# Kernel tuning notes

Measured on AMD Instinct MI355X. Metric: run time of the kernel, lower is better.

## Reference

```python
import jax, jax.numpy as jnp
import numpy as np

HEADS = 8
DIM_HEAD = 64
BOTTLENECK = 40


def setup_inputs() -> dict:
    key = jax.random.key(0)
    ks = jax.random.split(key, 10)
    b, n, qs = 4, 1024, 256
    inner = HEADS * DIM_HEAD
    s = lambda fan_in: 1.0 / np.sqrt(fan_in)
    return {
        "x":   jax.random.normal(ks[0], (b, n, qs), dtype=jnp.float32),
        # weights stored as (in, out) so forward is x @ W
        "wq1": jax.random.normal(ks[1], (qs, BOTTLENECK), dtype=jnp.float32) * s(qs),
        "wq2": jax.random.normal(ks[2], (BOTTLENECK, inner), dtype=jnp.float32) * s(BOTTLENECK),
        "wk1": jax.random.normal(ks[3], (qs, BOTTLENECK), dtype=jnp.float32) * s(qs),
        "wk2": jax.random.normal(ks[4], (BOTTLENECK, inner), dtype=jnp.float32) * s(BOTTLENECK),
        "wv1": jax.random.normal(ks[5], (qs, BOTTLENECK), dtype=jnp.float32) * s(qs),
        "wv2": jax.random.normal(ks[6], (BOTTLENECK, inner), dtype=jnp.float32) * s(BOTTLENECK),
        "wo":  jax.random.normal(ks[7], (inner, qs), dtype=jnp.float32) * s(inner),
        "bo":  jax.random.normal(ks[8], (qs,), dtype=jnp.float32) * 0.01,
    }


def reference(x, wq1, wq2, wk1, wk2, wv1, wv2, wo, bo):
    b, n, _ = x.shape
    h, d = HEADS, DIM_HEAD
    scale = d ** -0.5

    # bottlenecked QKV projections (40-dim), SiLU on K bottleneck
    q = (x @ wq1) @ wq2                       # (b, n, h*d)
    k = jax.nn.silu(x @ wk1) @ wk2            # (b, n, h*d)
    v = (x @ wv1) @ wv2                       # (b, n, h*d)

    def split(t):  # 'b n (h d) -> b (h n) d'
        return t.reshape(b, n, h, d).transpose(0, 2, 1, 3).reshape(b, h * n, d)

    q, k, v = split(q), split(k), split(v)

    sim = jnp.einsum('bid,bjd->bij', q, k) * scale   # (b, h*n, h*n)
    attn = jax.nn.softmax(sim, axis=-1)
    out = jnp.einsum('bij,bjd->bid', attn, v)        # (b, h*n, d)

    # 'b (h n) d -> b n (h d)'
    out = out.reshape(b, h, n, d).transpose(0, 2, 1, 3).reshape(b, n, h * d)
    return out @ wo + bo
```

## Files before the change

kernel.cpp:

```cpp
#include <hip/hip_runtime.h>
#include <hip/hip_bf16.h>


#define B_    4
#define H_    8
#define NSEQ  1024
#define SEQ   8192
#define DH    64
#define QS    256
#define INNER 512
#define QSCALE 0.18033688011112042f

#define KVSW_BATCH 524288
#define OPHALF (2097152)

typedef __bf16 bf16x8 __attribute__((ext_vector_type(8)));
typedef float floatx4 __attribute__((ext_vector_type(4)));

__global__ __launch_bounds__(512, 4) void qkv_kernel(
    const float* __restrict__ x,
    const float* __restrict__ wq1, const float* __restrict__ wq2,
    const float* __restrict__ wk1, const float* __restrict__ wk2,
    const float* __restrict__ wv1, const float* __restrict__ wv2,
    const float* __restrict__ wo,
    __hip_bfloat16* __restrict__ Qg, __hip_bfloat16* __restrict__ KSg,
    __hip_bfloat16* __restrict__ VSg,
    __hip_bfloat16* __restrict__ WOBH, __hip_bfloat16* __restrict__ WOBL)
{
  const int tid  = threadIdx.x;

  if (blockIdx.x >= 768) {
    const int cid = blockIdx.x - 768;
    const int t4  = (cid * 512 + tid) * 4;
    const int n   = t4 & 255;
    const int k8  = t4 >> 8;
    float4 rr[8];
    #pragma unroll
    for (int kk = 0; kk < 8; ++kk)
      rr[kk] = *(const float4*)(wo + (size_t)(k8 * 8 + kk) * QS + n);
    const int kc = k8 >> 2, qq = k8 & 3;
    #pragma unroll
    for (int nn = 0; nn < 4; ++nn) {
      const int nc = n + nn;
      const int l  = (nc & 15) + 16 * qq;
      const size_t off = ((size_t)((nc >> 4) * 16 + kc) * 64 + l) * 8;
      bf16x8 hv, lv;
      #pragma unroll
      for (int kk = 0; kk < 8; ++kk) {
        const float v = (nn == 0) ? rr[kk].x : (nn == 1) ? rr[kk].y
                      : (nn == 2) ? rr[kk].z : rr[kk].w;
        const __bf16 h16 = (__bf16)v;
        hv[kk] = h16;
        lv[kk] = (__bf16)(v - (float)h16);
      }
      *(bf16x8*)(WOBH + off) = hv;
      *(bf16x8*)(WOBL + off) = lv;
    }
    return;
  }

  const int p    = blockIdx.x >> 8;
  const int rest = blockIdx.x & 255;
  const int b    = rest >> 6;
  const int nblk = rest & 63;
  const int n0   = nblk << 4;

  __shared__ __align__(16) float xs[16][260];
  __shared__ __align__(16) float tb2[4][16][40];
  __shared__ __align__(16) float tb[16][40];
  __shared__ __align__(16) __hip_bfloat16 ob[10400];

  const float* w1 = (p == 0) ? wq1 : (p == 1) ? wk1 : wv1;
  const float* w2 = (p == 0) ? wq2 : (p == 1) ? wk2 : wv2;

  #pragma unroll
  for (int j = 0; j < 2; ++j) {
    const int i  = tid + j * 512;
    const int r  = i >> 6;
    const int c4 = (i & 63) << 2;
    *(float4*)(&xs[r][c4]) =
        *(const float4*)(x + ((size_t)b * NSEQ + n0 + r) * QS + c4);
  }
  __syncthreads();

  for (int t = tid; t < 640; t += 512) {
    const int ks  = t / 160;
    const int rem = t - ks * 160;
    const int r   = rem / 10;
    const int bn  = (rem - r * 10) * 4;
    float a0 = 0.f, a1 = 0.f, a2 = 0.f, a3 = 0.f;
    #pragma unroll 4
    for (int c4 = ks * 16; c4 < ks * 16 + 16; ++c4) {
      const float4 xv = *(const float4*)(&xs[r][c4 * 4]);
      const float4 wa = *(const float4*)(w1 + (c4 * 4 + 0) * 40 + bn);
      const float4 wb = *(const float4*)(w1 + (c4 * 4 + 1) * 40 + bn);
      const float4 wc = *(const float4*)(w1 + (c4 * 4 + 2) * 40 + bn);
      const float4 wd = *(const float4*)(w1 + (c4 * 4 + 3) * 40 + bn);
      a0 += xv.x * wa.x + xv.y * wb.x + xv.z * wc.x + xv.w * wd.x;
      a1 += xv.x * wa.y + xv.y * wb.y + xv.z * wc.y + xv.w * wd.y;
      a2 += xv.x * wa.z + xv.y * wb.z + xv.z * wc.z + xv.w * wd.z;
      a3 += xv.x * wa.w + xv.y * wb.w + xv.z * wc.w + xv.w * wd.w;
    }
    tb2[ks][r][bn + 0] = a0; tb2[ks][r][bn + 1] = a1;
    tb2[ks][r][bn + 2] = a2; tb2[ks][r][bn + 3] = a3;
  }
  __syncthreads();

  if (tid < 160) {
    const int r  = tid / 10;
    const int bn = (tid - r * 10) * 4;
    const float4 h0 = *(const float4*)(&tb2[0][r][bn]);
    const float4 h1 = *(const float4*)(&tb2[1][r][bn]);
    const float4 h2 = *(const float4*)(&tb2[2][r][bn]);
    const float4 h3 = *(const float4*)(&tb2[3][r][bn]);
    float a0 = (h0.x + h1.x) + (h2.x + h3.x);
    float a1 = (h0.y + h1.y) + (h2.y + h3.y);
    float a2 = (h0.z + h1.z) + (h2.z + h3.z);
    float a3 = (h0.w + h1.w) + (h2.w + h3.w);
    if (p == 1) {
      a0 = a0 / (1.f + __expf(-a0));
      a1 = a1 / (1.f + __expf(-a1));
      a2 = a2 / (1.f + __expf(-a2));
      a3 = a3 / (1.f + __expf(-a3));
    }
    tb[r][bn + 0] = a0; tb[r][bn + 1] = a1;
    tb[r][bn + 2] = a2; tb[r][bn + 3] = a3;
  }
  __syncthreads();

  {
    const int cq = tid & 127;
    const int rq = tid >> 7;
    const int c  = cq * 4, r0 = rq * 4;
    const float scale = (p == 0) ? QSCALE : 1.0f;
    float acc[4][4];
    #pragma unroll
    for (int i = 0; i < 4; ++i)
      #pragma unroll
      for (int j = 0; j < 4; ++j) acc[i][j] = 0.f;

    #pragma unroll 2
    for (int jb = 0; jb < 10; ++jb) {
      const float4 w0  = *(const float4*)(w2 + (jb * 4 + 0) * INNER + c);
      const float4 w1r = *(const float4*)(w2 + (jb * 4 + 1) * INNER + c);
      const float4 w2r = *(const float4*)(w2 + (jb * 4 + 2) * INNER + c);
      const float4 w3  = *(const float4*)(w2 + (jb * 4 + 3) * INNER + c);
      #pragma unroll
      for (int ri = 0; ri < 4; ++ri) {
        const float4 tv = *(const float4*)(&tb[r0 + ri][jb * 4]);
        acc[ri][0] += tv.x * w0.x + tv.y * w1r.x + tv.z * w2r.x + tv.w * w3.x;
        acc[ri][1] += tv.x * w0.y + tv.y * w1r.y + tv.z * w2r.y + tv.w * w3.y;
        acc[ri][2] += tv.x * w0.z + tv.y * w1r.z + tv.z * w2r.z + tv.w * w3.z;
        acc[ri][3] += tv.x * w0.w + tv.y * w1r.w + tv.z * w2r.w + tv.w * w3.w;
      }
    }
    #pragma unroll
    for (int ri = 0; ri < 4; ++ri)
      #pragma unroll
      for (int ci = 0; ci < 4; ++ci) {
        const int cc = c + ci;
        const float v = acc[ri][ci] * scale;
        if (p == 2) ob[cc * 20 + r0 + ri]    = __float2bfloat16(v);
        else        ob[(r0 + ri) * 520 + cc] = __float2bfloat16(v);
      }
  }
  __syncthreads();

  if (p == 0) {
    #pragma unroll
    for (int j = 0; j < 2; ++j) {
      const int i  = tid + j * 512;
      const int h  = i >> 7;
      const int r  = (i >> 3) & 15;
      const int d8 = i & 7;
      *(float4*)(Qg + ((size_t)b * SEQ + h * NSEQ + n0 + r) * DH + d8 * 8) =
          *(const float4*)(&ob[r * 520 + h * 64 + d8 * 8]);
    }
  } else if (p == 1) {
    #pragma unroll
    for (int j = 0; j < 2; ++j) {
      const int i    = tid + j * 512;
      const int h    = i >> 7;
      const int ks2  = (i >> 6) & 1;
      const int quad = (i >> 4) & 3;
      const int r    = i & 15;
      const int lane = quad * 16 + r;
      const size_t dst = (size_t)b * KVSW_BATCH
          + ((size_t)((h * 64 + nblk) * 2 + ks2) * 64 + lane) * 8;
      *(float4*)(KSg + dst) = *(const float4*)(&ob[r * 520 + h * 64 + ks2 * 32 + quad * 8]);
    }
  } else {
    const int st  = nblk & 1;
    const int p32 = nblk >> 1;
    #pragma unroll
    for (int pass = 0; pass < 4; ++pass) {
      const int i   = tid + pass * 512;
      const int h   = i >> 8;
      const int dnt = (i >> 6) & 3;
      const int dm  = (i >> 2) & 15;
      const int rg  = i & 3;
      const int lane = rg * 16 + dm;
      const size_t dst = (size_t)b * KVSW_BATCH
          + ((size_t)((h * 32 + p32) * 4 + dnt) * 64 + lane) * 8 + st * 4;
      *(uint2*)(VSg + dst) = *(const uint2*)(&ob[(h * 64 + dnt * 16 + dm) * 20 + rg * 4]);
    }
  }
}

struct PairBuf {
  bf16x8 k[2][2];
  bf16x8 v[4];
};

__global__ __launch_bounds__(256, 3) void attn_kernel(
    const __hip_bfloat16* __restrict__ Qg,
    const __hip_bfloat16* __restrict__ KSg,
    const __hip_bfloat16* __restrict__ VSg,
    float* __restrict__ OPg,
    float* __restrict__ PSg)
{
  __shared__ float Osh[4][16][68];
  __shared__ float psums[4][64];

  const int tid  = threadIdx.x;
  const int wave = tid >> 6;
  const int lane = tid & 63;
  const int lrow = lane & 15;
  const int quad = lane >> 4;

  const int xcd   = blockIdx.x & 7;
  const int idx   = blockIdx.x >> 3;
  const int b     = xcd >> 1;
  const int half  = idx & 1;
  const int qtile = (xcd & 1) * 64 + (idx >> 1);
  const int qbase = qtile * 64;

  const __hip_bfloat16* Qb  = Qg + ((size_t)b * SEQ + qbase) * DH;
  const __hip_bfloat16* kp0 = KSg + (size_t)b * KVSW_BATCH + half * 262144
                              + (size_t)wave * 65536 + lane * 8;
  const __hip_bfloat16* vp0 = VSg + (size_t)b * KVSW_BATCH + half * 262144
                              + (size_t)wave * 65536 + lane * 8;

  bf16x8 qf[4][2];
  #pragma unroll
  for (int mt = 0; mt < 4; ++mt)
    #pragma unroll
    for (int s = 0; s < 2; ++s)
      qf[mt][s] = *(const bf16x8*)(Qb + (mt * 16 + lrow) * DH + s * 32 + quad * 8);

  floatx4 oacc[4][4];
  #pragma unroll
  for (int mt = 0; mt < 4; ++mt)
    #pragma unroll
    for (int dnt = 0; dnt < 4; ++dnt)
      oacc[mt][dnt] = (floatx4){0.f, 0.f, 0.f, 0.f};
  float psum[4] = {0.f, 0.f, 0.f, 0.f};

  #pragma unroll 2
  for (int pair = 0; pair < 32; ++pair) {
    PairBuf pb;
    const __hip_bfloat16* kp = kp0 + pair * 2048;
    pb.k[0][0] = *(const bf16x8*)(kp);
    pb.k[0][1] = *(const bf16x8*)(kp + 512);
    pb.k[1][0] = *(const bf16x8*)(kp + 1024);
    pb.k[1][1] = *(const bf16x8*)(kp + 1536);
    const __hip_bfloat16* vp = vp0 + pair * 2048;
    #pragma unroll
    for (int dnt = 0; dnt < 4; ++dnt)
      pb.v[dnt] = *(const bf16x8*)(vp + dnt * 512);

    #pragma unroll
    for (int mt = 0; mt < 4; ++mt) {
      floatx4 s0 = (floatx4){0.f, 0.f, 0.f, 0.f};
      floatx4 s1 = (floatx4){0.f, 0.f, 0.f, 0.f};
      s0 = __builtin_amdgcn_mfma_f32_16x16x32_bf16(pb.k[0][0], qf[mt][0], s0, 0, 0, 0);
      s0 = __builtin_amdgcn_mfma_f32_16x16x32_bf16(pb.k[0][1], qf[mt][1], s0, 0, 0, 0);
      s1 = __builtin_amdgcn_mfma_f32_16x16x32_bf16(pb.k[1][0], qf[mt][0], s1, 0, 0, 0);
      s1 = __builtin_amdgcn_mfma_f32_16x16x32_bf16(pb.k[1][1], qf[mt][1], s1, 0, 0, 0);
      float p[8];
      #pragma unroll
      for (int r = 0; r < 4; ++r) {
        p[r]     = __builtin_amdgcn_exp2f(s0[r]);
        p[4 + r] = __builtin_amdgcn_exp2f(s1[r]);
      }
      psum[mt] += ((p[0] + p[1]) + (p[2] + p[3])) + ((p[4] + p[5]) + (p[6] + p[7]));
      bf16x8 pa;
      #pragma unroll
      for (int j = 0; j < 8; ++j) pa[j] = (__bf16)p[j];
      #pragma unroll
      for (int dnt = 0; dnt < 4; ++dnt)
        oacc[mt][dnt] = __builtin_amdgcn_mfma_f32_16x16x32_bf16(pa, pb.v[dnt], oacc[mt][dnt], 0, 0, 0);
    }
  }

  #pragma unroll
  for (int mt = 0; mt < 4; ++mt) {
    float s = psum[mt];
    s += __shfl_xor(s, 16, 64);
    s += __shfl_xor(s, 32, 64);
    psum[mt] = s;
  }
  if (quad == 0) {
    #pragma unroll
    for (int mt = 0; mt < 4; ++mt)
      psums[wave][mt * 16 + lrow] = psum[mt];
  }

  const size_t opbase = ((size_t)half * B_ + b) * SEQ + qbase;

  #pragma unroll
  for (int mt = 0; mt < 4; ++mt) {
    #pragma unroll
    for (int dnt = 0; dnt < 4; ++dnt)
      #pragma unroll
      for (int r = 0; r < 4; ++r)
        Osh[wave][quad * 4 + r][dnt * 16 + lrow] = oacc[mt][dnt][r];
    __syncthreads();

    {
      const int q16 = tid >> 4;
      const int d0  = (tid & 15) * 4;
      float4 a0 = *(const float4*)(&Osh[0][q16][d0]);
      float4 a1 = *(const float4*)(&Osh[1][q16][d0]);
      float4 a2 = *(const float4*)(&Osh[2][q16][d0]);
      float4 a3 = *(const float4*)(&Osh[3][q16][d0]);
      float4 res;
      res.x = (a0.x + a1.x) + (a2.x + a3.x);
      res.y = (a0.y + a1.y) + (a2.y + a3.y);
      res.z = (a0.z + a1.z) + (a2.z + a3.z);
      res.w = (a0.w + a1.w) + (a2.w + a3.w);
      *(float4*)(OPg + (opbase + mt * 16 + q16) * DH + d0) = res;
    }
    if (mt == 0 && tid < 64) {
      const float tot = (psums[0][tid] + psums[1][tid]) + (psums[2][tid] + psums[3][tid]);
      PSg[opbase + tid] = tot;
    }
    __syncthreads();
  }
}

__global__ __launch_bounds__(256, 1) void out_kernel(
    const float* __restrict__ OPg, const float* __restrict__ PSg,
    const __hip_bfloat16* __restrict__ WOBH, const __hip_bfloat16* __restrict__ WOBL,
    const float* __restrict__ bo, float* __restrict__ out)
{
  __shared__ __align__(16) __hip_bfloat16 apH[8192];
  __shared__ __align__(16) __hip_bfloat16 apL[8192];
  __shared__ float invs[16][8];

  const int tid  = threadIdx.x;
  const int b    = blockIdx.x >> 6;
  const int n0   = (blockIdx.x & 63) << 4;
  const int lane = tid & 63;
  const int wave = tid >> 6;

  if (tid < 128) {
    const int r = tid >> 3, h = tid & 7;
    const size_t row = (size_t)b * SEQ + h * NSEQ + n0 + r;
    invs[r][h] = 1.0f / (PSg[row] + PSg[(size_t)B_ * SEQ + row]);
  }
  __syncthreads();

  {
    const int m   = tid & 15;
    const int q   = (tid >> 4) & 3;
    const int kc0 = tid >> 6;
    #pragma unroll
    for (int pss = 0; pss < 4; ++pss) {
      const int kc = kc0 + pss * 4;
      const int h  = kc >> 1;
      const int dh = (q + 4 * (kc & 1)) * 8;
      const size_t idx = (((size_t)b * H_ + h) * NSEQ + n0 + m) * DH + dh;
      const float4 a0 = *(const float4*)(OPg + idx);
      const float4 a1 = *(const float4*)(OPg + idx + 4);
      const float4 b0 = *(const float4*)(OPg + OPHALF + idx);
      const float4 b1 = *(const float4*)(OPg + OPHALF + idx + 4);
      const float inv = invs[m][h];
      float v[8];
      v[0] = (a0.x + b0.x) * inv; v[1] = (a0.y + b0.y) * inv;
      v[2] = (a0.z + b0.z) * inv; v[3] = (a0.w + b0.w) * inv;
      v[4] = (a1.x + b1.x) * inv; v[5] = (a1.y + b1.y) * inv;
      v[6] = (a1.z + b1.z) * inv; v[7] = (a1.w + b1.w) * inv;
      bf16x8 hv, lv;
      #pragma unroll
      for (int j = 0; j < 8; ++j) {
        const __bf16 h16 = (__bf16)v[j];
        hv[j] = h16;
        lv[j] = (__bf16)(v[j] - (float)h16);
      }
      const int off = (kc * 64 + (m + 16 * q)) * 8;
      *(bf16x8*)(apH + off) = hv;
      *(bf16x8*)(apL + off) = lv;
    }
  }
  __syncthreads();

  bf16x8 ah[16], al[16];
  #pragma unroll
  for (int kc = 0; kc < 16; ++kc) {
    ah[kc] = *(const bf16x8*)(apH + (kc * 64 + lane) * 8);
    al[kc] = *(const bf16x8*)(apL + (kc * 64 + lane) * 8);
  }

  const int colq = lane & 15;
  const int quad = lane >> 4;

  #pragma unroll
  for (int nt4 = 0; nt4 < 4; ++nt4) {
    const int nt = nt4 * 4 + wave;
    const __hip_bfloat16* wbh = WOBH + ((size_t)nt * 16 * 64 + lane) * 8;
    const __hip_bfloat16* wbl = WOBL + ((size_t)nt * 16 * 64 + lane) * 8;
    floatx4 aHH = (floatx4){0.f, 0.f, 0.f, 0.f};
    floatx4 aHL = (floatx4){0.f, 0.f, 0.f, 0.f};
    floatx4 aLH = (floatx4){0.f, 0.f, 0.f, 0.f};
    #pragma unroll
    for (int kg = 0; kg < 4; ++kg) {
      bf16x8 bh[4], bl[4];
      #pragma unroll
      for (int j = 0; j < 4; ++j) {
        bh[j] = *(const bf16x8*)(wbh + (kg * 4 + j) * 512);
        bl[j] = *(const bf16x8*)(wbl + (kg * 4 + j) * 512);
      }
      #pragma unroll
      for (int j = 0; j < 4; ++j) {
        const int kc = kg * 4 + j;
        aHH = __builtin_amdgcn_mfma_f32_16x16x32_bf16(ah[kc], bh[j], aHH, 0, 0, 0);
        aHL = __builtin_amdgcn_mfma_f32_16x16x32_bf16(ah[kc], bl[j], aHL, 0, 0, 0);
        aLH = __builtin_amdgcn_mfma_f32_16x16x32_bf16(al[kc], bh[j], aLH, 0, 0, 0);
      }
    }
    const int n  = nt * 16 + colq;
    const float bv = bo[n];
    #pragma unroll
    for (int r = 0; r < 4; ++r) {
      const int mm = quad * 4 + r;
      out[((size_t)b * NSEQ + n0 + mm) * QS + n] =
          ((aHH[r] + aHL[r]) + aLH[r]) + bv;
    }
  }
}

extern "C" void kernel_launch(void* const* d_in, const int* in_sizes, int n_in,
                              void* d_out, int out_size, void* d_ws, size_t ws_size,
                              hipStream_t stream) {
  const float* x   = (const float*)d_in[0];
  const float* wq1 = (const float*)d_in[1];
  const float* wq2 = (const float*)d_in[2];
  const float* wk1 = (const float*)d_in[3];
  const float* wk2 = (const float*)d_in[4];
  const float* wv1 = (const float*)d_in[5];
  const float* wv2 = (const float*)d_in[6];
  const float* wo  = (const float*)d_in[7];
  const float* bo  = (const float*)d_in[8];
  float* out = (float*)d_out;

  __hip_bfloat16* Qg  = (__hip_bfloat16*)d_ws;
  __hip_bfloat16* KSg = Qg + (size_t)B_ * SEQ * DH;
  __hip_bfloat16* VSg = KSg + (size_t)B_ * KVSW_BATCH;
  float*          OPg = (float*)(VSg + (size_t)B_ * KVSW_BATCH);
  float*          PSg = OPg + 2 * (size_t)B_ * SEQ * DH;
  __hip_bfloat16* WOBH = (__hip_bfloat16*)(PSg + 2 * (size_t)B_ * SEQ);
  __hip_bfloat16* WOBL = WOBH + (size_t)INNER * QS;

  qkv_kernel<<<776, 512, 0, stream>>>(x, wq1, wq2, wk1, wk2, wv1, wv2, wo,
                                      Qg, KSg, VSg, WOBH, WOBL);
  attn_kernel<<<1024, 256, 0, stream>>>(Qg, KSg, VSg, OPg, PSg);
  out_kernel<<<256, 256, 0, stream>>>(OPg, PSg, WOBH, WOBL, bo, out);
}
```

Baseline: 179.9 us.

## Move QKV bottleneck projections to split-bf16 MFMA with fused Q/K/V blocks

The QKV projection now runs both stages of the bottleneck GEMMs on bf16 MFMA instructions. A 3-term hi/lo split (hh + hl + lh) keeps accuracy close to fp32. A new conv_kernel converts all weight matrices into swizzled hi/lo bf16 layouts ahead of time. Each qkv block now computes Q, K and V together for its 16 rows, so x is loaded once instead of three times, and the grid drops from 768 to 256 blocks. The cost is an extra kernel launch and MFMA-layout overhead on very small matrices (40-wide bottleneck padded to 64), and fewer blocks means less parallelism.

```diff
diff --git a/kernel.cpp b/kernel.cpp
--- a/kernel.cpp
+++ b/kernel.cpp
@@ -17,21 +17,62 @@
 typedef __bf16 bf16x8 __attribute__((ext_vector_type(8)));
 typedef float floatx4 __attribute__((ext_vector_type(4)));
 
-__global__ __launch_bounds__(512, 4) void qkv_kernel(
-    const float* __restrict__ x,
-    const float* __restrict__ wq1, const float* __restrict__ wq2,
-    const float* __restrict__ wk1, const float* __restrict__ wk2,
-    const float* __restrict__ wv1, const float* __restrict__ wv2,
+__global__ __launch_bounds__(256) void conv_kernel(
+    const float* __restrict__ wq1, const float* __restrict__ wk1,
+    const float* __restrict__ wv1,
+    const float* __restrict__ wq2, const float* __restrict__ wk2,
+    const float* __restrict__ wv2,
     const float* __restrict__ wo,
-    __hip_bfloat16* __restrict__ Qg, __hip_bfloat16* __restrict__ KSg,
-    __hip_bfloat16* __restrict__ VSg,
+    __hip_bfloat16* __restrict__ W1BH, __hip_bfloat16* __restrict__ W1BL,
+    __hip_bfloat16* __restrict__ W2BH, __hip_bfloat16* __restrict__ W2BL,
     __hip_bfloat16* __restrict__ WOBH, __hip_bfloat16* __restrict__ WOBL)
 {
-  const int tid  = threadIdx.x;
-
-  if (blockIdx.x >= 768) {
-    const int cid = blockIdx.x - 768;
-    const int t4  = (cid * 512 + tid) * 4;
+  const int tid = threadIdx.x;
+  const int blk = blockIdx.x;
+
+  if (blk < 16) {
+    const int t  = blk * 256 + tid;
+    const int n  = t & 127;
+    const int kq = t >> 7;
+    const int kc = kq >> 2, q = kq & 3;
+    const float* src; int col;
+    if (n < 40)       { src = wq1; col = n; }
+    else if (n < 80)  { src = wk1; col = n - 40; }
+    else if (n < 120) { src = wv1; col = n - 80; }
+    else              { src = nullptr; col = 0; }
+    bf16x8 hv, lv;
+    #pragma unroll
+    for (int j = 0; j < 8; ++j) {
+      const int k = kc * 32 + q * 8 + j;
+      const float v = src ? src[k * 40 + col] : 0.f;
+      const __bf16 h16 = (__bf16)v;
+      hv[j] = h16; lv[j] = (__bf16)(v - (float)h16);
+    }
+    const size_t off = (((size_t)(n >> 4) * 8 + kc) * 64 + (n & 15) + 16 * q) * 8;
+    *(bf16x8*)(W1BH + off) = hv;
+    *(bf16x8*)(W1BL + off) = lv;
+  } else if (blk < 64) {
+    const int t  = (blk - 16) * 256 + tid;
+    const int n  = t & 511;
+    const int r  = t >> 9;
+    const int p  = r >> 3;
+    const int kq = r & 7;
+    const int kc = kq >> 2, q = kq & 3;
+    const float* w2 = (p == 0) ? wq2 : (p == 1) ? wk2 : wv2;
+    bf16x8 hv, lv;
+    #pragma unroll
+    for (int j = 0; j < 8; ++j) {
+      const int k = kc * 32 + q * 8 + j;
+      const float v = (k < 40) ? w2[(size_t)k * 512 + n] : 0.f;
+      const __bf16 h16 = (__bf16)v;
+      hv[j] = h16; lv[j] = (__bf16)(v - (float)h16);
+    }
+    const size_t off = ((((size_t)p * 32 + (n >> 4)) * 2 + kc) * 64 + (n & 15) + 16 * q) * 8;
+    *(bf16x8*)(W2BH + off) = hv;
+    *(bf16x8*)(W2BL + off) = lv;
+  } else {
+    const int cid = blk - 64;
+    const int t4  = (cid * 256 + tid) * 4;
     const int n   = t4 & 255;
     const int k8  = t4 >> 8;
     float4 rr[8];
@@ -56,22 +97,30 @@
       *(bf16x8*)(WOBH + off) = hv;
       *(bf16x8*)(WOBL + off) = lv;
     }
-    return;
-  }
-
-  const int p    = blockIdx.x >> 8;
-  const int rest = blockIdx.x & 255;
-  const int b    = rest >> 6;
-  const int nblk = rest & 63;
+  }
+}
+
+__global__ __launch_bounds__(512) void qkv_kernel(
+    const float* __restrict__ x,
+    const __hip_bfloat16* __restrict__ W1BH, const __hip_bfloat16* __restrict__ W1BL,
+    const __hip_bfloat16* __restrict__ W2BH, const __hip_bfloat16* __restrict__ W2BL,
+    __hip_bfloat16* __restrict__ Qg, __hip_bfloat16* __restrict__ KSg,
+    __hip_bfloat16* __restrict__ VSg)
+{
+  const int tid  = threadIdx.x;
+  const int b    = blockIdx.x >> 6;
+  const int nblk = blockIdx.x & 63;
   const int n0   = nblk << 4;
+  const int wave = tid >> 6;
+  const int lane = tid & 63;
+  const int m    = lane & 15;
+  const int q    = lane >> 4;
 
   __shared__ __align__(16) float xs[16][260];
-  __shared__ __align__(16) float tb2[4][16][40];
-  __shared__ __align__(16) float tb[16][40];
-  __shared__ __align__(16) __hip_bfloat16 ob[10400];
-
-  const float* w1 = (p == 0) ? wq1 : (p == 1) ? wk1 : wv1;
-  const float* w2 = (p == 0) ? wq2 : (p == 1) ? wk2 : wv2;
+  __shared__ __align__(16) float tb32[16][140];
+  __shared__ __align__(16) __hip_bfloat16 qb[8320];
+  __shared__ __align__(16) __hip_bfloat16 kb[8320];
+  __shared__ __align__(16) __hip_bfloat16 vb[10240];
 
   #pragma unroll
   for (int j = 0; j < 2; ++j) {
@@ -83,113 +132,123 @@
   }
   __syncthreads();
 
-  for (int t = tid; t < 640; t += 512) {
-    const int ks  = t / 160;
-    const int rem = t - ks * 160;
-    const int r   = rem / 10;
-    const int bn  = (rem - r * 10) * 4;
-    float a0 = 0.f, a1 = 0.f, a2 = 0.f, a3 = 0.f;
-    #pragma unroll 4
-    for (int c4 = ks * 16; c4 < ks * 16 + 16; ++c4) {
-      const float4 xv = *(const float4*)(&xs[r][c4 * 4]);
-      const float4 wa = *(const float4*)(w1 + (c4 * 4 + 0) * 40 + bn);
-      const float4 wb = *(const float4*)(w1 + (c4 * 4 + 1) * 40 + bn);
-      const float4 wc = *(const float4*)(w1 + (c4 * 4 + 2) * 40 + bn);
-      const float4 wd = *(const float4*)(w1 + (c4 * 4 + 3) * 40 + bn);
-      a0 += xv.x * wa.x + xv.y * wb.x + xv.z * wc.x + xv.w * wd.x;
-      a1 += xv.x * wa.y + xv.y * wb.y + xv.z * wc.y + xv.w * wd.y;
-      a2 += xv.x * wa.z + xv.y * wb.z + xv.z * wc.z + xv.w * wd.z;
-      a3 += xv.x * wa.w + xv.y * wb.w + xv.z * wc.w + xv.w * wd.w;
-    }
-    tb2[ks][r][bn + 0] = a0; tb2[ks][r][bn + 1] = a1;
-    tb2[ks][r][bn + 2] = a2; tb2[ks][r][bn + 3] = a3;
+  bf16x8 xh[8], xl[8];
+  #pragma unroll
+  for (int kc = 0; kc < 8; ++kc) {
+    const float4 f0 = *(const float4*)(&xs[m][kc * 32 + q * 8]);
+    const float4 f1 = *(const float4*)(&xs[m][kc * 32 + q * 8 + 4]);
+    float v[8] = {f0.x, f0.y, f0.z, f0.w, f1.x, f1.y, f1.z, f1.w};
+    #pragma unroll
+    for (int j = 0; j < 8; ++j) {
+      const __bf16 h16 = (__bf16)v[j];
+      xh[kc][j] = h16;
+      xl[kc][j] = (__bf16)(v[j] - (float)h16);
+    }
+  }
+
+  {
+    floatx4 hh = (floatx4){0.f, 0.f, 0.f, 0.f};
+    floatx4 hl = (floatx4){0.f, 0.f, 0.f, 0.f};
+    floatx4 lh = (floatx4){0.f, 0.f, 0.f, 0.f};
+    const __hip_bfloat16* w1h = W1BH + ((size_t)wave * 8 * 64 + lane) * 8;
+    const __hip_bfloat16* w1l = W1BL + ((size_t)wave * 8 * 64 + lane) * 8;
+    #pragma unroll
+    for (int kc = 0; kc < 8; ++kc) {
+      const bf16x8 bh = *(const bf16x8*)(w1h + kc * 512);
+      const bf16x8 bl = *(const bf16x8*)(w1l + kc * 512);
+      hh = __builtin_amdgcn_mfma_f32_16x16x32_bf16(xh[kc], bh, hh, 0, 0, 0);
+      hl = __builtin_amdgcn_mfma_f32_16x16x32_bf16(xh[kc], bl, hl, 0, 0, 0);
+      lh = __builtin_amdgcn_mfma_f32_16x16x32_bf16(xl[kc], bh, lh, 0, 0, 0);
+    }
+    const int n1 = wave * 16 + m;
+    #pragma unroll
+    for (int r = 0; r < 4; ++r) {
+      float d = (hh[r] + hl[r]) + lh[r];
+      if (n1 >= 40 && n1 < 80) d = d / (1.f + __expf(-d));
+      tb32[q * 4 + r][n1] = d;
+    }
   }
   __syncthreads();
 
-  if (tid < 160) {
-    const int r  = tid / 10;
-    const int bn = (tid - r * 10) * 4;
-    const float4 h0 = *(const float4*)(&tb2[0][r][bn]);
-    const float4 h1 = *(const float4*)(&tb2[1][r][bn]);
-    const float4 h2 = *(const float4*)(&tb2[2][r][bn]);
-    const float4 h3 = *(const float4*)(&tb2[3][r][bn]);
-    float a0 = (h0.x + h1.x) + (h2.x + h3.x);
-    float a1 = (h0.y + h1.y) + (h2.y + h3.y);
-    float a2 = (h0.z + h1.z) + (h2.z + h3.z);
-    float a3 = (h0.w + h1.w) + (h2.w + h3.w);
-    if (p == 1) {
-      a0 = a0 / (1.f + __expf(-a0));
-      a1 = a1 / (1.f + __expf(-a1));
-      a2 = a2 / (1.f + __expf(-a2));
-      a3 = a3 / (1.f + __expf(-a3));
-    }
-    tb[r][bn + 0] = a0; tb[r][bn + 1] = a1;
-    tb[r][bn + 2] = a2; tb[r][bn + 3] = a3;
+  #pragma unroll
+  for (int p = 0; p < 3; ++p) {
+    bf16x8 a2h[2], a2l[2];
+    {
+      const float4 g0 = *(const float4*)(&tb32[m][p * 40 + q * 8]);
+      const float4 g1 = *(const float4*)(&tb32[m][p * 40 + q * 8 + 4]);
+      float v[8] = {g0.x, g0.y, g0.z, g0.w, g1.x, g1.y, g1.z, g1.w};
+      #pragma unroll
+      for (int j = 0; j < 8; ++j) {
+        const __bf16 h16 = (__bf16)v[j];
+        a2h[0][j] = h16;
+        a2l[0][j] = (__bf16)(v[j] - (float)h16);
+      }
+    }
+    if (q == 0) {
+      const float4 g0 = *(const float4*)(&tb32[m][p * 40 + 32]);
+      const float4 g1 = *(const float4*)(&tb32[m][p * 40 + 36]);
+      float v[8] = {g0.x, g0.y, g0.z, g0.w, g1.x, g1.y, g1.z, g1.w};
+      #pragma unroll
+      for (int j = 0; j < 8; ++j) {
+        const __bf16 h16 = (__bf16)v[j];
+        a2h[1][j] = h16;
+        a2l[1][j] = (__bf16)(v[j] - (float)h16);
+      }
+    } else {
+      #pragma unroll
+      for (int j = 0; j < 8; ++j) { a2h[1][j] = (__bf16)0.f; a2l[1][j] = (__bf16)0.f; }
+    }
+
+    #pragma unroll
+    for (int i = 0; i < 4; ++i) {
+      const int nt = wave * 4 + i;
+      floatx4 sHH = (floatx4){0.f, 0.f, 0.f, 0.f};
+      floatx4 sHL = (floatx4){0.f, 0.f, 0.f, 0.f};
+      floatx4 sLH = (floatx4){0.f, 0.f, 0.f, 0.f};
+      #pragma unroll
+      for (int kc = 0; kc < 2; ++kc) {
+        const size_t boff = (((size_t)(p * 32 + nt) * 2 + kc) * 64 + lane) * 8;
+        const bf16x8 bh = *(const bf16x8*)(W2BH + boff);
+        const bf16x8 bl = *(const bf16x8*)(W2BL + boff);
+        sHH = __builtin_amdgcn_mfma_f32_16x16x32_bf16(a2h[kc], bh, sHH, 0, 0, 0);
+        sHL = __builtin_amdgcn_mfma_f32_16x16x32_bf16(a2h[kc], bl, sHL, 0, 0, 0);
+        sLH = __builtin_amdgcn_mfma_f32_16x16x32_bf16(a2l[kc], bh, sLH, 0, 0, 0);
+      }
+      const int nn = nt * 16 + m;
+      #pragma unroll
+      for (int r = 0; r < 4; ++r) {
+        const int row = q * 4 + r;
+        const float d = (sHH[r] + sHL[r]) + sLH[r];
+        if (p == 0)      qb[row * 520 + nn] = __float2bfloat16(d * QSCALE);
+        else if (p == 1) kb[row * 520 + nn] = __float2bfloat16(d);
+        else             vb[nn * 20 + row]  = __float2bfloat16(d);
+      }
+    }
   }
   __syncthreads();
 
+  #pragma unroll
+  for (int j = 0; j < 2; ++j) {
+    const int i  = tid + j * 512;
+    const int h  = i >> 7;
+    const int r  = (i >> 3) & 15;
+    const int d8 = i & 7;
+    *(float4*)(Qg + ((size_t)b * SEQ + h * NSEQ + n0 + r) * DH + d8 * 8) =
+        *(const float4*)(&qb[r * 520 + h * 64 + d8 * 8]);
+  }
+  #pragma unroll
+  for (int j = 0; j < 2; ++j) {
+    const int i    = tid + j * 512;
+    const int h    = i >> 7;
+    const int ks2  = (i >> 6) & 1;
+    const int quad = (i >> 4) & 3;
+    const int r    = i & 15;
+    const int ln   = quad * 16 + r;
+    const size_t dst = (size_t)b * KVSW_BATCH
+        + ((size_t)((h * 64 + nblk) * 2 + ks2) * 64 + ln) * 8;
+    *(float4*)(KSg + dst) = *(const float4*)(&kb[r * 520 + h * 64 + ks2 * 32 + quad * 8]);
+  }
   {
-    const int cq = tid & 127;
-    const int rq = tid >> 7;
-    const int c  = cq * 4, r0 = rq * 4;
-    const float scale = (p == 0) ? QSCALE : 1.0f;
-    float acc[4][4];
-    #pragma unroll
-    for (int i = 0; i < 4; ++i)
-      #pragma unroll
-      for (int j = 0; j < 4; ++j) acc[i][j] = 0.f;
-
-    #pragma unroll 2
-    for (int jb = 0; jb < 10; ++jb) {
-      const float4 w0  = *(const float4*)(w2 + (jb * 4 + 0) * INNER + c);
-      const float4 w1r = *(const float4*)(w2 + (jb * 4 + 1) * INNER + c);
-      const float4 w2r = *(const float4*)(w2 + (jb * 4 + 2) * INNER + c);
-      const float4 w3  = *(const float4*)(w2 + (jb * 4 + 3) * INNER + c);
-      #pragma unroll
-      for (int ri = 0; ri < 4; ++ri) {
-        const float4 tv = *(const float4*)(&tb[r0 + ri][jb * 4]);
-        acc[ri][0] += tv.x * w0.x + tv.y * w1r.x + tv.z * w2r.x + tv.w * w3.x;
-        acc[ri][1] += tv.x * w0.y + tv.y * w1r.y + tv.z * w2r.y + tv.w * w3.y;
-        acc[ri][2] += tv.x * w0.z + tv.y * w1r.z + tv.z * w2r.z + tv.w * w3.z;
-        acc[ri][3] += tv.x * w0.w + tv.y * w1r.w + tv.z * w2r.w + tv.w * w3.w;
-      }
-    }
-    #pragma unroll
-    for (int ri = 0; ri < 4; ++ri)
-      #pragma unroll
-      for (int ci = 0; ci < 4; ++ci) {
-        const int cc = c + ci;
-        const float v = acc[ri][ci] * scale;
-        if (p == 2) ob[cc * 20 + r0 + ri]    = __float2bfloat16(v);
-        else        ob[(r0 + ri) * 520 + cc] = __float2bfloat16(v);
-      }
-  }
-  __syncthreads();
-
-  if (p == 0) {
-    #pragma unroll
-    for (int j = 0; j < 2; ++j) {
-      const int i  = tid + j * 512;
-      const int h  = i >> 7;
-      const int r  = (i >> 3) & 15;
-      const int d8 = i & 7;
-      *(float4*)(Qg + ((size_t)b * SEQ + h * NSEQ + n0 + r) * DH + d8 * 8) =
-          *(const float4*)(&ob[r * 520 + h * 64 + d8 * 8]);
-    }
-  } else if (p == 1) {
-    #pragma unroll
-    for (int j = 0; j < 2; ++j) {
-      const int i    = tid + j * 512;
-      const int h    = i >> 7;
-      const int ks2  = (i >> 6) & 1;
-      const int quad = (i >> 4) & 3;
-      const int r    = i & 15;
-      const int lane = quad * 16 + r;
-      const size_t dst = (size_t)b * KVSW_BATCH
-          + ((size_t)((h * 64 + nblk) * 2 + ks2) * 64 + lane) * 8;
-      *(float4*)(KSg + dst) = *(const float4*)(&ob[r * 520 + h * 64 + ks2 * 32 + quad * 8]);
-    }
-  } else {
     const int st  = nblk & 1;
     const int p32 = nblk >> 1;
     #pragma unroll
@@ -199,10 +258,10 @@
       const int dnt = (i >> 6) & 3;
       const int dm  = (i >> 2) & 15;
       const int rg  = i & 3;
-      const int lane = rg * 16 + dm;
+      const int ln  = rg * 16 + dm;
       const size_t dst = (size_t)b * KVSW_BATCH
-          + ((size_t)((h * 32 + p32) * 4 + dnt) * 64 + lane) * 8 + st * 4;
-      *(uint2*)(VSg + dst) = *(const uint2*)(&ob[(h * 64 + dnt * 16 + dm) * 20 + rg * 4]);
+          + ((size_t)((h * 32 + p32) * 4 + dnt) * 64 + ln) * 8 + st * 4;
+      *(uint2*)(VSg + dst) = *(const uint2*)(&vb[(h * 64 + dnt * 16 + dm) * 20 + rg * 4]);
     }
   }
 }
@@ -461,9 +520,14 @@
   float*          PSg = OPg + 2 * (size_t)B_ * SEQ * DH;
   __hip_bfloat16* WOBH = (__hip_bfloat16*)(PSg + 2 * (size_t)B_ * SEQ);
   __hip_bfloat16* WOBL = WOBH + (size_t)INNER * QS;
-
-  qkv_kernel<<<776, 512, 0, stream>>>(x, wq1, wq2, wk1, wk2, wv1, wv2, wo,
-                                      Qg, KSg, VSg, WOBH, WOBL);
+  __hip_bfloat16* W1BH = WOBL + (size_t)INNER * QS;
+  __hip_bfloat16* W1BL = W1BH + 32768;
+  __hip_bfloat16* W2BH = W1BL + 32768;
+  __hip_bfloat16* W2BL = W2BH + 98304;
+
+  conv_kernel<<<80, 256, 0, stream>>>(wq1, wk1, wv1, wq2, wk2, wv2, wo,
+                                      W1BH, W1BL, W2BH, W2BL, WOBH, WOBL);
+  qkv_kernel<<<256, 512, 0, stream>>>(x, W1BH, W1BL, W2BH, W2BL, Qg, KSg, VSg);
   attn_kernel<<<1024, 256, 0, stream>>>(Qg, KSg, VSg, OPg, PSg);
   out_kernel<<<256, 256, 0, stream>>>(OPg, PSg, WOBH, WOBL, bo, out);
 }
```

After: 166.0 us, median of 2. -7.8%, faster.
